# Performance work log

Measured on AMD Instinct MI355X. Metric: run time of the kernel, lower is better.

Reference implementation:

```python
import jax, jax.numpy as jnp
import numpy as np

SPARSITY = 0.15
GAIN = 3.0

def setup_inputs() -> dict:
    key = jax.random.key(0)
    x = jax.random.normal(key, (16384, 4096), dtype=jnp.float32)
    return {"x": x}

def reference(x):
    N, D = x.shape
    k = max(int(D * SPARSITY), 2)
    topk_values, topk_indices = jax.lax.top_k(x, k)  # [N, k]
    diff = topk_values[:, 0] - topk_values[:, 1]      # [N]
    dynamic_gain = (jax.nn.sigmoid(diff) * GAIN + 1.0)[:, None]  # [N, 1]
    rows = jnp.arange(N)[:, None]
    mask = jnp.zeros_like(x).at[rows, topk_indices].set(1.0)
    return x * mask * dynamic_gain
```

## Files before the change

kernel.cpp:

```cpp
#include <hip/hip_runtime.h>
#include <math.h>


#define D     4096
#define K     614
#define BLOCK 256
#define VPT   64
#define NB    16

typedef float f32x4 __attribute__((ext_vector_type(4)));

__device__ __forceinline__ unsigned int f2ord(float f) {
    unsigned int b = __float_as_uint(f);
    return ((int)b >= 0) ? (b | 0x80000000u) : ~b;
}
__device__ __forceinline__ float ord2f(unsigned int u) {
    return __uint_as_float(((int)u < 0) ? (u ^ 0x80000000u) : ~u);
}

__global__ __launch_bounds__(BLOCK, 4)
void diffgated_topk(const float* __restrict__ x, float* __restrict__ out, int rows) {
    const int lane = threadIdx.x & 63;
    const int wav  = threadIdx.x >> 6;
    const int row  = blockIdx.x * 4 + wav;
    if (row >= rows) return;
    const f32x4* xrow = (const f32x4*)(x + (size_t)row * D);
    f32x4*       orow = (f32x4*)(out + (size_t)row * D);

    const unsigned int A = f2ord(0.90f);
    const unsigned int B = f2ord(1.17f);

    unsigned int u[VPT];
    unsigned int m1 = 0u, m2 = 0u;
    unsigned int cab = 0u;
    #pragma unroll
    for (int b = 0; b < NB; ++b) {
        f32x4 v = xrow[b * 64 + lane];
        #pragma unroll
        for (int j = 0; j < 4; ++j) {
            unsigned int q = f2ord(v[j]);
            unsigned int lo2 = min(m1, q);
            m1 = max(m1, q);
            m2 = max(m2, lo2);
            cab += (q >= A) ? 1u : 0u;
            cab += (q >= B) ? 0x10000u : 0u;
            u[b * 4 + j] = q;
        }
    }

    #pragma unroll
    for (int off = 32; off; off >>= 1) {
        unsigned int o1 = __shfl_xor(m1, off);
        unsigned int o2 = __shfl_xor(m2, off);
        cab += __shfl_xor(cab, off);
        unsigned int hi2 = max(m1, o1), lo2 = min(m1, o1);
        m2 = max(m2, max(lo2, o2));
        m1 = hi2;
    }
    const int cnt_a = (int)(cab & 0xFFFFu);
    const int cnt_b = (int)(cab >> 16);
    const float gain = 3.0f / (1.0f + expf(-(ord2f(m1) - ord2f(m2)))) + 1.0f;

    unsigned long long lo, hi;
    int cnt_lo, cnt_hi;
    if (cnt_a >= K) {
        if (cnt_b >= K) { lo = B; cnt_lo = cnt_b; hi = 0x100000000ull; cnt_hi = 0; }
        else            { lo = A; cnt_lo = cnt_a; hi = B;              cnt_hi = cnt_b; }
    } else              { lo = 0; cnt_lo = D;     hi = A;              cnt_hi = cnt_a; }

    int toggle = 0;
    while (hi - lo > 1ull && cnt_lo != K) {
        unsigned long long span = hi - lo;
        unsigned long long mid;
        if (toggle) {
            mid = lo + (span >> 1);
        } else {
            float frac = (float)(cnt_lo - K) *
                         __builtin_amdgcn_rcpf((float)(cnt_lo - cnt_hi));
            unsigned long long step = (unsigned long long)((float)span * frac);
            if (step < 1ull)        step = 1ull;
            if (step > span - 1ull) step = span - 1ull;
            mid = lo + step;
        }
        toggle ^= 1;
        const unsigned int midu = (unsigned int)mid;
        int cnt = 0;
        #pragma unroll
        for (int j = 0; j < VPT; ++j)
            cnt += (int)__popcll(__ballot(u[j] >= midu));
        if (cnt >= K) { lo = mid; cnt_lo = cnt; }
        else          { hi = mid; cnt_hi = cnt; }
    }
    const unsigned int ut = (unsigned int)lo;
    const float g = gain;

    if (cnt_lo == K) {
        #pragma unroll
        for (int b = 0; b < NB; ++b) {
            f32x4 o;
            #pragma unroll
            for (int j = 0; j < 4; ++j) {
                unsigned int uu = u[b * 4 + j];
                o[j] = (uu >= ut) ? ord2f(uu) * g : 0.0f;
            }
            __builtin_nontemporal_store(o, orow + b * 64 + lane);
        }
    } else {
        const int needed = K - cnt_hi;
        const unsigned long long ltmask =
            (lane == 0) ? 0ull : ((~0ull) >> (64 - lane));
        int eq_before = 0;
        #pragma unroll
        for (int b = 0; b < NB; ++b) {
            unsigned long long bal[4];
            #pragma unroll
            for (int j = 0; j < 4; ++j) bal[j] = __ballot(u[b * 4 + j] == ut);
            f32x4 o;
            #pragma unroll
            for (int j = 0; j < 4; ++j) {
                unsigned int uu = u[b * 4 + j];
                float f = 0.0f;
                if (uu > ut) {
                    f = ord2f(uu) * g;
                } else if (uu == ut) {
                    int r = eq_before;
                    #pragma unroll
                    for (int j2 = 0; j2 < 4; ++j2) {
                        r += (int)__popcll(bal[j2] & ltmask);
                        if (j2 < j) r += (int)((bal[j2] >> lane) & 1ull);
                    }
                    if (r < needed) f = ord2f(uu) * g;
                }
                o[j] = f;
            }
            __builtin_nontemporal_store(o, orow + b * 64 + lane);
            #pragma unroll
            for (int j2 = 0; j2 < 4; ++j2)
                eq_before += (int)__popcll(bal[j2]);
        }
    }
}

extern "C" void kernel_launch(void* const* d_in, const int* in_sizes, int n_in,
                              void* d_out, int out_size, void* d_ws, size_t ws_size,
                              hipStream_t stream) {
    const float* x = (const float*)d_in[0];
    float* out = (float*)d_out;
    const int rows = in_sizes[0] / D;
    diffgated_topk<<<dim3((rows + 3) / 4), dim3(BLOCK), 0, stream>>>(x, out, rows);
}
```

Before: 457.6 us.

## Split each row across a whole block instead of one wavefront

Each 4096-element row is now handled by a 256-thread block (4 waves) rather than a single wave, so each thread keeps 16 values in registers instead of 64. Max, second-max and counts are combined across waves through shared memory, and every bisection step needs a __syncthreads. The fast path also compares raw floats in the positive [0.90, 1.17] bracket, which avoids the order-preserving integer conversion. The aim is lower register pressure and higher occupancy (launch bounds go from 4 to 8), paid for with a block barrier on every search iteration.

```diff
diff --git a/kernel.cpp b/kernel.cpp
--- a/kernel.cpp
+++ b/kernel.cpp
@@ -5,8 +5,8 @@
 #define D     4096
 #define K     614
 #define BLOCK 256
-#define VPT   64
-#define NB    16
+#define NW    4
+#define NB    4
 
 typedef float f32x4 __attribute__((ext_vector_type(4)));
 
@@ -14,129 +14,199 @@
     unsigned int b = __float_as_uint(f);
     return ((int)b >= 0) ? (b | 0x80000000u) : ~b;
 }
-__device__ __forceinline__ float ord2f(unsigned int u) {
-    return __uint_as_float(((int)u < 0) ? (u ^ 0x80000000u) : ~u);
-}
-
-__global__ __launch_bounds__(BLOCK, 4)
+
+__global__ __launch_bounds__(BLOCK, 8)
 void diffgated_topk(const float* __restrict__ x, float* __restrict__ out, int rows) {
-    const int lane = threadIdx.x & 63;
-    const int wav  = threadIdx.x >> 6;
-    const int row  = blockIdx.x * 4 + wav;
-    if (row >= rows) return;
+    const int tid  = threadIdx.x;
+    const int lane = tid & 63;
+    const int w    = tid >> 6;
+    const int row  = blockIdx.x;
     const f32x4* xrow = (const f32x4*)(x + (size_t)row * D);
     f32x4*       orow = (f32x4*)(out + (size_t)row * D);
 
-    const unsigned int A = f2ord(0.90f);
-    const unsigned int B = f2ord(1.17f);
-
-    unsigned int u[VPT];
-    unsigned int m1 = 0u, m2 = 0u;
+    __shared__ float        sm1[NW], sm2[NW];
+    __shared__ unsigned int scab[NW];
+    __shared__ int          scnt[2][NW];
+    __shared__ int          eqc[NB][NW];
+
+    const float A = 0.90f, B = 1.17f;
+
+    f32x4 vv[NB];
+    float m1 = -INFINITY, m2 = -INFINITY;
     unsigned int cab = 0u;
     #pragma unroll
     for (int b = 0; b < NB; ++b) {
-        f32x4 v = xrow[b * 64 + lane];
+        f32x4 v = xrow[b * 256 + tid];
+        vv[b] = v;
         #pragma unroll
         for (int j = 0; j < 4; ++j) {
-            unsigned int q = f2ord(v[j]);
-            unsigned int lo2 = min(m1, q);
-            m1 = max(m1, q);
-            m2 = max(m2, lo2);
+            float q = v[j];
+            float lo2 = fminf(m1, q);
+            m1 = fmaxf(m1, q);
+            m2 = fmaxf(m2, lo2);
             cab += (q >= A) ? 1u : 0u;
             cab += (q >= B) ? 0x10000u : 0u;
-            u[b * 4 + j] = q;
         }
     }
 
     #pragma unroll
     for (int off = 32; off; off >>= 1) {
-        unsigned int o1 = __shfl_xor(m1, off);
-        unsigned int o2 = __shfl_xor(m2, off);
+        float o1 = __shfl_xor(m1, off);
+        float o2 = __shfl_xor(m2, off);
         cab += __shfl_xor(cab, off);
-        unsigned int hi2 = max(m1, o1), lo2 = min(m1, o1);
-        m2 = max(m2, max(lo2, o2));
+        float hi2 = fmaxf(m1, o1), lo2 = fminf(m1, o1);
+        m2 = fmaxf(m2, fmaxf(lo2, o2));
         m1 = hi2;
+    }
+
+    if (lane == 0) { sm1[w] = m1; sm2[w] = m2; scab[w] = cab; }
+    __syncthreads();
+    {
+        float a1 = sm1[0], a2 = sm2[0];
+        unsigned int c = scab[0];
+        #pragma unroll
+        for (int i = 1; i < NW; ++i) {
+            float b1 = sm1[i], b2 = sm2[i];
+            float n1 = fmaxf(a1, b1);
+            float n2 = fmaxf(fminf(a1, b1), fmaxf(a2, b2));
+            a1 = n1; a2 = n2; c += scab[i];
+        }
+        m1 = a1; m2 = a2; cab = c;
     }
     const int cnt_a = (int)(cab & 0xFFFFu);
     const int cnt_b = (int)(cab >> 16);
-    const float gain = 3.0f / (1.0f + expf(-(ord2f(m1) - ord2f(m2)))) + 1.0f;
-
-    unsigned long long lo, hi;
+    const float gain = 3.0f / (1.0f + expf(-(m1 - m2))) + 1.0f;
+
+    unsigned int ut_ord;
     int cnt_lo, cnt_hi;
-    if (cnt_a >= K) {
-        if (cnt_b >= K) { lo = B; cnt_lo = cnt_b; hi = 0x100000000ull; cnt_hi = 0; }
-        else            { lo = A; cnt_lo = cnt_a; hi = B;              cnt_hi = cnt_b; }
-    } else              { lo = 0; cnt_lo = D;     hi = A;              cnt_hi = cnt_a; }
-
-    int toggle = 0;
-    while (hi - lo > 1ull && cnt_lo != K) {
-        unsigned long long span = hi - lo;
-        unsigned long long mid;
-        if (toggle) {
-            mid = lo + (span >> 1);
-        } else {
-            float frac = (float)(cnt_lo - K) *
-                         __builtin_amdgcn_rcpf((float)(cnt_lo - cnt_hi));
-            unsigned long long step = (unsigned long long)((float)span * frac);
-            if (step < 1ull)        step = 1ull;
-            if (step > span - 1ull) step = span - 1ull;
-            mid = lo + step;
-        }
-        toggle ^= 1;
-        const unsigned int midu = (unsigned int)mid;
-        int cnt = 0;
-        #pragma unroll
-        for (int j = 0; j < VPT; ++j)
-            cnt += (int)__popcll(__ballot(u[j] >= midu));
-        if (cnt >= K) { lo = mid; cnt_lo = cnt; }
-        else          { hi = mid; cnt_hi = cnt; }
-    }
-    const unsigned int ut = (unsigned int)lo;
-    const float g = gain;
-
-    if (cnt_lo == K) {
-        #pragma unroll
-        for (int b = 0; b < NB; ++b) {
-            f32x4 o;
-            #pragma unroll
-            for (int j = 0; j < 4; ++j) {
-                unsigned int uu = u[b * 4 + j];
-                o[j] = (uu >= ut) ? ord2f(uu) * g : 0.0f;
-            }
-            __builtin_nontemporal_store(o, orow + b * 64 + lane);
-        }
+
+    if (cnt_a >= K && cnt_b < K) {
+        unsigned int lo = __float_as_uint(A), hi = __float_as_uint(B);
+        cnt_lo = cnt_a; cnt_hi = cnt_b;
+        int it = 0;
+        while (hi - lo > 1u && cnt_lo != K) {
+            unsigned int span = hi - lo;
+            unsigned int mid;
+            if (it & 1) {
+                mid = lo + (span >> 1);
+            } else {
+                float frac = (float)(cnt_lo - K) *
+                             __builtin_amdgcn_rcpf((float)(cnt_lo - cnt_hi));
+                unsigned int step = (unsigned int)((float)span * frac);
+                if (step < 1u)        step = 1u;
+                if (step > span - 1u) step = span - 1u;
+                mid = lo + step;
+            }
+            const float midf = __uint_as_float(mid);
+            int cw = 0;
+            #pragma unroll
+            for (int b = 0; b < NB; ++b)
+                #pragma unroll
+                for (int j = 0; j < 4; ++j)
+                    cw += (int)__popcll(__ballot(vv[b][j] >= midf));
+            const int p = it & 1;
+            if (lane == 0) scnt[p][w] = cw;
+            __syncthreads();
+            int cnt = scnt[p][0] + scnt[p][1] + scnt[p][2] + scnt[p][3];
+            if (cnt >= K) { lo = mid; cnt_lo = cnt; }
+            else          { hi = mid; cnt_hi = cnt; }
+            ++it;
+        }
+        if (cnt_lo == K) {
+            const float tf = __uint_as_float(lo);
+            #pragma unroll
+            for (int b = 0; b < NB; ++b) {
+                f32x4 o;
+                #pragma unroll
+                for (int j = 0; j < 4; ++j) {
+                    float q = vv[b][j];
+                    o[j] = (q >= tf) ? q * gain : 0.0f;
+                }
+                __builtin_nontemporal_store(o, orow + b * 256 + tid);
+            }
+            return;
+        }
+        ut_ord = lo | 0x80000000u;
     } else {
+        unsigned long long lo = 0ull, hi = 0x100000000ull;
+        cnt_lo = D; cnt_hi = 0;
+        int it = 0;
+        while (hi - lo > 1ull && cnt_lo != K) {
+            unsigned int mid = (unsigned int)((lo + hi) >> 1);
+            int cw = 0;
+            for (int b = 0; b < NB; ++b)
+                for (int j = 0; j < 4; ++j)
+                    cw += (int)__popcll(__ballot(f2ord(vv[b][j]) >= mid));
+            const int p = it & 1;
+            if (lane == 0) scnt[p][w] = cw;
+            __syncthreads();
+            int cnt = scnt[p][0] + scnt[p][1] + scnt[p][2] + scnt[p][3];
+            if (cnt >= K) { lo = mid; cnt_lo = cnt; }
+            else          { hi = mid; cnt_hi = cnt; }
+            ++it;
+        }
+        ut_ord = (unsigned int)lo;
+        if (cnt_lo == K) {
+            #pragma unroll
+            for (int b = 0; b < NB; ++b) {
+                f32x4 o;
+                #pragma unroll
+                for (int j = 0; j < 4; ++j) {
+                    float q = vv[b][j];
+                    o[j] = (f2ord(q) >= ut_ord) ? q * gain : 0.0f;
+                }
+                __builtin_nontemporal_store(o, orow + b * 256 + tid);
+            }
+            return;
+        }
+    }
+
+    {
         const int needed = K - cnt_hi;
         const unsigned long long ltmask =
             (lane == 0) ? 0ull : ((~0ull) >> (64 - lane));
-        int eq_before = 0;
         #pragma unroll
         for (int b = 0; b < NB; ++b) {
+            int e = 0;
+            #pragma unroll
+            for (int j = 0; j < 4; ++j)
+                e += (int)__popcll(__ballot(f2ord(vv[b][j]) == ut_ord));
+            if (lane == 0) eqc[b][w] = e;
+        }
+        __syncthreads();
+        int base = 0;
+        #pragma unroll
+        for (int b = 0; b < NB; ++b) {
+            int pre = base;
+            for (int wp = 0; wp < w; ++wp) pre += eqc[b][wp];
             unsigned long long bal[4];
             #pragma unroll
-            for (int j = 0; j < 4; ++j) bal[j] = __ballot(u[b * 4 + j] == ut);
+            for (int j = 0; j < 4; ++j)
+                bal[j] = __ballot(f2ord(vv[b][j]) == ut_ord);
             f32x4 o;
             #pragma unroll
             for (int j = 0; j < 4; ++j) {
-                unsigned int uu = u[b * 4 + j];
+                float q = vv[b][j];
+                unsigned int uo = f2ord(q);
                 float f = 0.0f;
-                if (uu > ut) {
-                    f = ord2f(uu) * g;
-                } else if (uu == ut) {
-                    int r = eq_before;
+                if (uo > ut_ord) {
+                    f = q * gain;
+                } else if (uo == ut_ord) {
+                    int r = pre;
                     #pragma unroll
                     for (int j2 = 0; j2 < 4; ++j2) {
                         r += (int)__popcll(bal[j2] & ltmask);
                         if (j2 < j) r += (int)((bal[j2] >> lane) & 1ull);
                     }
-                    if (r < needed) f = ord2f(uu) * g;
+                    if (r < needed) f = q * gain;
                 }
                 o[j] = f;
             }
-            __builtin_nontemporal_store(o, orow + b * 64 + lane);
-            #pragma unroll
-            for (int j2 = 0; j2 < 4; ++j2)
-                eq_before += (int)__popcll(bal[j2]);
+            __builtin_nontemporal_store(o, orow + b * 256 + tid);
+            int tot = 0;
+            #pragma unroll
+            for (int wp = 0; wp < NW; ++wp) tot += eqc[b][wp];
+            base += tot;
         }
     }
 }
@@ -147,5 +217,5 @@
     const float* x = (const float*)d_in[0];
     float* out = (float*)d_out;
     const int rows = in_sizes[0] / D;
-    diffgated_topk<<<dim3((rows + 3) / 4), dim3(BLOCK), 0, stream>>>(x, out, rows);
+    diffgated_topk<<<dim3(rows), dim3(BLOCK), 0, stream>>>(x, out, rows);
 }
```

Result: faster. 445.1 us (-2.7%).
